# Kernel optimization log

Measured on AMD Instinct MI355X. Metric: run time of the kernel, lower is better.

## Reference

```python
import jax, jax.numpy as jnp
import numpy as np

E = 576        # embed_dims
HEADS = 18
NPTS = 12
NF = 3         # num_frames
DD = 2 * NF - 1  # depth of value volume (5)
HD = E // HEADS  # head dim (32)


def _grid_init_bias():
    # Faithful reproduction of init_weights() for sampling_offsets.bias
    theta = np.arange(8) * (2.0 * np.pi / 8)
    yaw = np.stack([np.cos(theta), np.sin(theta), np.zeros(8)], -1)
    roll = np.stack([np.zeros(8), np.cos(theta), np.sin(theta)], -1)
    pitch = np.stack([np.cos(theta), np.zeros(8), np.sin(theta)], -1)
    g = np.concatenate([yaw, pitch[[1, 2, 3, 5, 6, 7]], roll[[1, 3, 5, 7]]], 0)  # (18,3)
    g = g / np.abs(g).max(-1, keepdims=True)
    g = np.tile(g[:, None, None, :], (1, 1, NPTS, 1))              # (18,1,12,3)
    g = g * np.arange(1, NPTS + 1, dtype=np.float64)[None, None, :, None]
    return g.reshape(-1).astype(np.float32)                        # (18*12*3,)


def setup_inputs() -> dict:
    key = jax.random.key(0)
    ks = jax.random.split(key, 6)
    bs, h, w = 2, 64, 80
    nq = h * w
    lim = float(np.sqrt(6.0 / (E + E)))  # xavier uniform for square E x E
    return {
        "query": jax.random.normal(ks[0], (bs, nq, E), jnp.float32),
        "value": jax.random.normal(ks[1], (bs, nq * DD, E), jnp.float32),
        "query_pos": jax.random.normal(ks[2], (bs, nq, E), jnp.float32),
        "W_off": jnp.zeros((E, HEADS * NPTS * 3), jnp.float32),  # constant_init 0
        "b_off": jnp.asarray(_grid_init_bias()),
        "W_attn": jnp.zeros((E, HEADS * NPTS), jnp.float32),
        "b_attn": jnp.zeros((HEADS * NPTS,), jnp.float32),
        "W_v": jax.random.uniform(ks[3], (E, E), jnp.float32, -lim, lim),
        "b_v": jnp.zeros((E,), jnp.float32),
        "W_out": jax.random.uniform(ks[4], (E, E), jnp.float32, -lim, lim),
        "b_out": jnp.zeros((E,), jnp.float32),
        "h": 64,
        "w": 80,
    }


def _deform_attn_3d(value, loc, attn, D, H, W):
    # value: (bs, D*H*W, heads, hd)  token order: depth-major (D, H, W)
    # loc:   (bs, nq, heads, np, 3)  normalized (x, y, z) in [0,1]
    # attn:  (bs, nq, heads, np)
    bs, _, heads, hd = value.shape
    nq = loc.shape[1]
    # (bs, heads, D*H*W, hd) flat spatial for gathers
    v = value.reshape(bs, D, H, W, heads, hd).transpose(0, 4, 1, 2, 3, 5)
    v = v.reshape(bs, heads, D * H * W, hd)
    lt = jnp.moveaxis(loc, 2, 1)    # (bs, heads, nq, np, 3)
    at = jnp.moveaxis(attn, 2, 1)   # (bs, heads, nq, np)
    # grid_sample(align_corners=False) coordinate convention: pix = u*size - 0.5
    x = lt[..., 0] * W - 0.5
    y = lt[..., 1] * H - 0.5
    z = lt[..., 2] * D - 0.5
    x0 = jnp.floor(x); y0 = jnp.floor(y); z0 = jnp.floor(z)
    fx = x - x0; fy = y - y0; fz = z - z0
    acc = jnp.zeros((bs, heads, nq, NPTS, hd), v.dtype)
    for dz in (0, 1):
        for dy in (0, 1):
            for dx in (0, 1):
                xi = x0 + dx; yi = y0 + dy; zi = z0 + dz
                wgt = ((fx if dx else 1.0 - fx)
                       * (fy if dy else 1.0 - fy)
                       * (fz if dz else 1.0 - fz))
                valid = ((xi >= 0) & (xi < W) & (yi >= 0) & (yi < H)
                         & (zi >= 0) & (zi < D))
                xc = jnp.clip(xi, 0, W - 1).astype(jnp.int32)
                yc = jnp.clip(yi, 0, H - 1).astype(jnp.int32)
                zc = jnp.clip(zi, 0, D - 1).astype(jnp.int32)
                idx = ((zc * H + yc) * W + xc).reshape(bs, heads, nq * NPTS)
                g = jnp.take_along_axis(v, idx[..., None], axis=2)
                g = g.reshape(bs, heads, nq, NPTS, hd)
                acc = acc + g * (wgt * valid.astype(v.dtype))[..., None]
    out = jnp.einsum("bhqp,bhqpd->bhqd", at, acc)  # softmax-weighted sum over points
    return out.transpose(0, 2, 1, 3).reshape(bs, nq, heads * hd)


def _forward(query, value, query_pos, W_off, b_off, W_attn, b_attn,
             W_v, b_v, W_out, b_out, h, w):
    bs, nq, _ = query.shape
    q = query + query_pos
    v = (value @ W_v + b_v).reshape(bs, nq * DD, HEADS, HD)
    offs = (q @ W_off + b_off).reshape(bs, nq, HEADS, NPTS, 3)
    attn = jax.nn.softmax((q @ W_attn + b_attn).reshape(bs, nq, HEADS, NPTS), axis=-1)
    # reference points: pixel centers normalized, z = 0
    ry, rx = jnp.meshgrid((jnp.arange(h, dtype=jnp.float32) + 0.5) / h,
                          (jnp.arange(w, dtype=jnp.float32) + 0.5) / w,
                          indexing="ij")
    ref = jnp.stack([rx.reshape(-1), ry.reshape(-1),
                     jnp.zeros(h * w, jnp.float32)], -1)  # (nq, 3)
    norm = jnp.array([w, h, NF], jnp.float32)  # NOTE: z normalized by num_frames (as in source)
    loc = ref[None, :, None, None, :] + offs / norm
    out = _deform_attn_3d(v, loc, attn, DD, h, w)
    return out @ W_out + b_out  # dropout is identity at eval


def reference(query, value, query_pos, W_off, b_off, W_attn, b_attn,
              W_v, b_v, W_out, b_out, h, w):
    return _forward(query, value, query_pos, W_off, b_off, W_attn, b_attn,
                    W_v, b_v, W_out, b_out, h, w)
```

## Files before the change

### kernel.cpp

```cpp
#include <hip/hip_runtime.h>
#include <cstdint>

#define E_DIM   576
#define HEADS   18
#define NPTS    12
#define DDEPTH  5
#define HDIM    32
#define BSZ     2
#define GH      64
#define GW      80
#define NQ      (GH*GW)
#define NTOK    (NQ*DDEPTH)
#define MIXW    864
#define BQ_TOT  (BSZ*NQ)

typedef __attribute__((ext_vector_type(8))) short short8;
typedef __attribute__((ext_vector_type(4))) float f32x4;

__device__ __forceinline__ float b2f_lo(uint32_t u) {
    union { uint32_t u; float f; } v; v.u = u << 16; return v.f;
}
__device__ __forceinline__ float b2f_hi(uint32_t u) {
    union { uint32_t u; float f; } v; v.u = u & 0xffff0000u; return v.f;
}
__device__ __forceinline__ ushort f2b(float f) {
    union { float f; uint32_t u; } v; v.f = f;
    return (ushort)((v.u + 0x7fffu + ((v.u >> 16) & 1u)) >> 16);
}

__global__ void prep_all(const float* __restrict__ value,
                         const float* __restrict__ query, const float* __restrict__ query_pos,
                         const float* __restrict__ W_v, const float* __restrict__ W_out,
                         const float* __restrict__ W_off, const float* __restrict__ W_attn,
                         const float* __restrict__ b_off, const float* __restrict__ b_attn,
                         ushort* __restrict__ val_bf16, ushort* __restrict__ q_bf16,
                         ushort* __restrict__ wt_v, ushort* __restrict__ wt_out,
                         ushort* __restrict__ wt_mix, float* __restrict__ bias_mix) {
    const int i = blockIdx.x * blockDim.x + threadIdx.x;
    if (i < 51200 * 576 / 4) {
        const float4 v = reinterpret_cast<const float4*>(value)[i];
        ushort4 o; o.x = f2b(v.x); o.y = f2b(v.y); o.z = f2b(v.z); o.w = f2b(v.w);
        reinterpret_cast<ushort4*>(val_bf16)[i] = o;
    }
    if (i < 10240 * 576 / 4) {
        const float4 va = reinterpret_cast<const float4*>(query)[i];
        const float4 vb = reinterpret_cast<const float4*>(query_pos)[i];
        ushort4 o;
        o.x = f2b(va.x + vb.x); o.y = f2b(va.y + vb.y);
        o.z = f2b(va.z + vb.z); o.w = f2b(va.w + vb.w);
        reinterpret_cast<ushort4*>(q_bf16)[i] = o;
    }
    if (i < 864) bias_mix[i] = (i < 648) ? b_off[i] : b_attn[i - 648];
    if (i < 331776) {
        int n = i / E_DIM, k = i - n * E_DIM;
        wt_v[i] = f2b(W_v[(size_t)k * E_DIM + n]);
    } else if (i < 663552) {
        int j = i - 331776;
        int n = j / E_DIM, k = j - n * E_DIM;
        wt_out[j] = f2b(W_out[(size_t)k * E_DIM + n]);
    } else if (i < 1161216) {
        int j = i - 663552;
        int n = j / E_DIM, k = j - n * E_DIM;
        float v = (n < 648) ? W_off[(size_t)k * 648 + n] : W_attn[(size_t)k * 216 + (n - 648)];
        wt_mix[j] = f2b(v);
    }
}

#define TM 128
#define TN 96
#define BK 32

__device__ __forceinline__ void async_cp16(const ushort* gsrc, ushort* ldst) {
    __builtin_amdgcn_global_load_lds(
        (const __attribute__((address_space(1))) void*)gsrc,
        (__attribute__((address_space(3))) void*)ldst, 16, 0, 0);
}

template <typename OutT>
__device__ __forceinline__ void gemm_body(ushort* __restrict__ smem, int bx, int by,
                                          const ushort* __restrict__ A,
                                          const ushort* __restrict__ Bt,
                                          const float* __restrict__ bias,
                                          OutT* __restrict__ C, int K, int ldc) {
    ushort* Asb = smem;
    ushort* Bsb = smem + TM * BK;
    const int tid  = threadIdx.x;
    const int wave = tid >> 6;
    const int lane = tid & 63;
    const int m16  = lane & 15;
    const int quad = lane >> 4;
    const int wr   = wave >> 1;
    const int wc   = wave & 1;
    const int row0 = bx * TM;
    const int n0   = by * TN;

    const f32x4 zero = {0.f, 0.f, 0.f, 0.f};
    f32x4 acc[4][3];
    #pragma unroll
    for (int rt = 0; rt < 4; ++rt)
        #pragma unroll
        for (int ct = 0; ct < 3; ++ct) acc[rt][ct] = zero;

    const int srow = lane >> 2;
    const int scol = (((lane & 3) ^ ((lane >> 3) & 3))) * 8;
    const int ksw  = (quad ^ ((m16 >> 1) & 3)) * 8;

    for (int k0 = 0; k0 < K; k0 += BK) {
        #pragma unroll
        for (int c = 0; c < 2; ++c) {
            const int ch = wave + c * 4;
            async_cp16(A + (size_t)(row0 + ch * 16 + srow) * K + k0 + scol,
                       Asb + ch * 512 + lane * 8);
        }
        async_cp16(Bt + (size_t)(n0 + wave * 16 + srow) * K + k0 + scol,
                   Bsb + wave * 512 + lane * 8);
        if (wave < 2)
            async_cp16(Bt + (size_t)(n0 + (wave + 4) * 16 + srow) * K + k0 + scol,
                       Bsb + (wave + 4) * 512 + lane * 8);
        __syncthreads();

        short8 afrag[4], bfrag[3];
        #pragma unroll
        for (int rt = 0; rt < 4; ++rt)
            afrag[rt] = *reinterpret_cast<const short8*>(
                Asb + (wr * 4 + rt) * 512 + m16 * 32 + ksw);
        #pragma unroll
        for (int ct = 0; ct < 3; ++ct)
            bfrag[ct] = *reinterpret_cast<const short8*>(
                Bsb + (wc * 3 + ct) * 512 + m16 * 32 + ksw);

        #pragma unroll
        for (int rt = 0; rt < 4; ++rt)
            #pragma unroll
            for (int ct = 0; ct < 3; ++ct)
                acc[rt][ct] = __builtin_amdgcn_mfma_f32_16x16x32_bf16(
                    afrag[rt], bfrag[ct], acc[rt][ct], 0, 0, 0);

        __syncthreads();
    }

    #pragma unroll
    for (int ct = 0; ct < 3; ++ct) {
        const int col = n0 + wc * 48 + ct * 16 + m16;
        const float bcol = bias[col];
        #pragma unroll
        for (int rt = 0; rt < 4; ++rt) {
            #pragma unroll
            for (int r = 0; r < 4; ++r) {
                const int row = row0 + wr * 64 + rt * 16 + quad * 4 + r;
                const float val = acc[rt][ct][r] + bcol;
                if constexpr (__is_same(OutT, float)) {
                    C[(size_t)row * ldc + col] = val;
                } else {
                    C[(size_t)row * ldc + col] = f2b(val);
                }
            }
        }
    }
}

template <typename OutT>
__global__ void gemm_mfma(const ushort* __restrict__ A, const ushort* __restrict__ Bt,
                          const float* __restrict__ bias, OutT* __restrict__ C,
                          int K, int ldc) {
    __shared__ __align__(16) ushort smem[(TM + TN) * BK];
    gemm_body<OutT>(smem, blockIdx.x, blockIdx.y, A, Bt, bias, C, K, ldc);
}

__global__ void gemm_dual(const ushort* __restrict__ A1, const ushort* __restrict__ B1,
                          const float* __restrict__ bias1, float* __restrict__ C1,
                          int K1, int ldc1, int nbx1, int split,
                          const ushort* __restrict__ A2, const ushort* __restrict__ B2,
                          const float* __restrict__ bias2, ushort* __restrict__ C2,
                          int K2, int ldc2, int nbx2) {
    __shared__ __align__(16) ushort smem[(TM + TN) * BK];
    const int id = blockIdx.x;
    if (id < split) {
        gemm_body<float>(smem, id % nbx1, id / nbx1, A1, B1, bias1, C1, K1, ldc1);
    } else {
        const int j = id - split;
        gemm_body<ushort>(smem, j % nbx2, j / nbx2, A2, B2, bias2, C2, K2, ldc2);
    }
}

__global__ void __launch_bounds__(256, 8)
deform_kernel(const ushort* __restrict__ vbuf,
              const float* __restrict__ mix,
              ushort* __restrict__ aout) {
    __shared__ uint2 corn[16 * NPTS * 8];
    __shared__ uint32_t cmask[16 * NPTS];
    const int gl   = threadIdx.x >> 4;
    const int l    = threadIdx.x & 15;
    const int head = blockIdx.x / 640;
    const int bq   = (blockIdx.x % 640) * 16 + gl;
    const int q    = bq % NQ;
    const int b    = bq / NQ;
    const int qx   = q % GW;
    const int qy   = q / GW;

    const float* mrow = mix + (size_t)bq * MIXW;

    float lg = (l < NPTS) ? mrow[648 + head * NPTS + l] : -1e30f;
    float mx = lg;
    #pragma unroll
    for (int mk = 1; mk < 16; mk <<= 1) mx = fmaxf(mx, __shfl_xor(mx, mk, 16));
    float e = (l < NPTS) ? __expf(lg - mx) : 0.f;
    float s = e;
    #pragma unroll
    for (int mk = 1; mk < 16; mk <<= 1) s += __shfl_xor(s, mk, 16);

    float    cw[8];
    uint32_t coff[8];
    uint32_t mask = 0;
    {
        const float ap = e / s;
        const int pl = (l < NPTS) ? l : 0;
        const int ob = (head * NPTS + pl) * 3;
        const float ox = mrow[ob + 0];
        const float oy = mrow[ob + 1];
        const float oz = mrow[ob + 2];
        const float x = (float)qx + ox;
        const float y = (float)qy + oy;
        const float z = oz * (5.0f / 3.0f) - 0.5f;
        const float x0f = floorf(x), y0f = floorf(y), z0f = floorf(z);
        const int x0 = (int)x0f, y0 = (int)y0f, z0 = (int)z0f;
        const float fx = x - x0f, fy = y - y0f, fz = z - z0f;

        #pragma unroll
        for (int dz = 0; dz < 2; ++dz) {
            const int zi = z0 + dz;
            const bool zv = (zi >= 0) & (zi < DDEPTH);
            const int zc = min(max(zi, 0), DDEPTH - 1);
            const float wz = dz ? fz : 1.f - fz;
            #pragma unroll
            for (int dy = 0; dy < 2; ++dy) {
                const int yi = y0 + dy;
                const bool yv = (yi >= 0) & (yi < GH);
                const int yc = min(max(yi, 0), GH - 1);
                const float wy = dy ? fy : 1.f - fy;
                #pragma unroll
                for (int dx = 0; dx < 2; ++dx) {
                    const int xi = x0 + dx;
                    const bool xv = (xi >= 0) & (xi < GW);
                    const int xc = min(max(xi, 0), GW - 1);
                    const float wx = dx ? fx : 1.f - fx;
                    const int i = dz * 4 + dy * 2 + dx;
                    const bool valid = zv & yv & xv & (l < NPTS);
                    cw[i]   = ap * wz * wy * wx;
                    coff[i] = (uint32_t)((zc * GH + yc) * GW + xc) * (E_DIM / 2);
                    mask |= (valid ? (1u << i) : 0u);
                }
            }
        }
    }

    if (l < NPTS) {
        cmask[gl * NPTS + l] = mask;
        uint4* dst = reinterpret_cast<uint4*>(&corn[(gl * NPTS + l) * 8]);
        #pragma unroll
        for (int i2 = 0; i2 < 4; ++i2) {
            uint4 w;
            w.x = __float_as_uint(cw[2 * i2]);     w.y = coff[2 * i2];
            w.z = __float_as_uint(cw[2 * i2 + 1]); w.w = coff[2 * i2 + 1];
            dst[i2] = w;
        }
    }
    __syncthreads();

    const uint32_t* vb = reinterpret_cast<const uint32_t*>(vbuf)
                         + (size_t)b * NTOK * (E_DIM / 2) + head * (HDIM / 2) + l;
    const uint2* cg = &corn[gl * NPTS * 8];
    float o0 = 0.f, o1 = 0.f;
    for (int p = 0; p < NPTS; ++p) {
        const uint32_t msk = cmask[gl * NPTS + p];
        if (msk == 0) continue;
        #pragma unroll
        for (int i = 0; i < 8; ++i) {
            if (msk & (1u << i)) {
                const uint2 wo = cg[p * 8 + i];
                const float w = __uint_as_float(wo.x);
                const uint32_t pair = vb[wo.y];
                o0 += w * b2f_lo(pair);
                o1 += w * b2f_hi(pair);
            }
        }
    }
    const uint32_t packed = (uint32_t)f2b(o0) | ((uint32_t)f2b(o1) << 16);
    reinterpret_cast<uint32_t*>(aout)[(size_t)bq * (E_DIM / 2) + head * (HDIM / 2) + l] = packed;
}

extern "C" void kernel_launch(void* const* d_in, const int* in_sizes, int n_in,
                              void* d_out, int out_size, void* d_ws, size_t ws_size,
                              hipStream_t stream) {
    const float* query     = (const float*)d_in[0];
    const float* value     = (const float*)d_in[1];
    const float* query_pos = (const float*)d_in[2];
    const float* W_off     = (const float*)d_in[3];
    const float* b_off     = (const float*)d_in[4];
    const float* W_attn    = (const float*)d_in[5];
    const float* b_attn    = (const float*)d_in[6];
    const float* W_v       = (const float*)d_in[7];
    const float* b_v       = (const float*)d_in[8];
    const float* W_out     = (const float*)d_in[9];
    const float* b_out     = (const float*)d_in[10];
    float* out = (float*)d_out;

    char* ws = (char*)d_ws;
    ushort* vbuf     = (ushort*)(ws);
    ushort* val_bf16 = (ushort*)(ws + 58982400);
    ushort* aout     = val_bf16;
    ushort* q_bf16   = (ushort*)(ws + 117964800);
    float*  mixb     = (float*) (ws + 129761280);
    ushort* wt_v     = (ushort*)(ws + 165150720);
    ushort* wt_out   = (ushort*)(ws + 165814272);
    ushort* wt_mix   = (ushort*)(ws + 166477824);
    float*  bias_mix = (float*) (ws + 167473152);

    prep_all<<<(51200 * 576 / 4) / 256, 256, 0, stream>>>(
        value, query, query_pos, W_v, W_out, W_off, W_attn, b_off, b_attn,
        val_bf16, q_bf16, wt_v, wt_out, wt_mix, bias_mix);

    gemm_dual<<<720 + 2400, 256, 0, stream>>>(
        q_bf16, wt_mix, bias_mix, mixb, E_DIM, MIXW, BQ_TOT / TM, 720,
        val_bf16, wt_v, b_v, vbuf, E_DIM, E_DIM, (BSZ * NTOK) / TM);

    deform_kernel<<<HEADS * 640, 256, 0, stream>>>(vbuf, mixb, aout);

    gemm_mfma<float><<<dim3(BQ_TOT / TM, E_DIM / TN), 256, 0, stream>>>(
        aout, wt_out, b_out, out, E_DIM, E_DIM);
}
```

Measured before the change: 396.1 us.

## Remap GEMM blocks per XCD and compact valid deform corners into dense list

GEMM block indices are remapped so that consecutive logical tiles, which share the same A row panel across N tiles, land on the same XCD. The goal is better L2 reuse on the multi-die GPU. The deform kernel now prefix-sums the per-point valid-corner counts across the 16 lanes and writes only valid corners into a compacted shared-memory list, so the gather loop runs over a dense count with no per-bit mask checks. The mapping assumes the total block count is divisible by 8, and the compaction adds shuffle work before the barrier.

```diff
diff --git a/kernel.cpp b/kernel.cpp
--- a/kernel.cpp
+++ b/kernel.cpp
@@ -74,6 +74,14 @@
     __builtin_amdgcn_global_load_lds(
         (const __attribute__((address_space(1))) void*)gsrc,
         (__attribute__((address_space(3))) void*)ldst, 16, 0, 0);
+}
+
+__device__ __forceinline__ void xcd_map(int id, int total, int nbn, int& bx, int& by) {
+    const int xcd = id & 7;
+    const int pos = id >> 3;
+    const int logical = xcd * (total >> 3) + pos;
+    by = logical % nbn;
+    bx = logical / nbn;
 }
 
 template <typename OutT>
@@ -162,24 +170,28 @@
 template <typename OutT>
 __global__ void gemm_mfma(const ushort* __restrict__ A, const ushort* __restrict__ Bt,
                           const float* __restrict__ bias, OutT* __restrict__ C,
-                          int K, int ldc) {
+                          int K, int ldc, int total, int nbn) {
     __shared__ __align__(16) ushort smem[(TM + TN) * BK];
-    gemm_body<OutT>(smem, blockIdx.x, blockIdx.y, A, Bt, bias, C, K, ldc);
+    int bx, by;
+    xcd_map(blockIdx.x, total, nbn, bx, by);
+    gemm_body<OutT>(smem, bx, by, A, Bt, bias, C, K, ldc);
 }
 
 __global__ void gemm_dual(const ushort* __restrict__ A1, const ushort* __restrict__ B1,
                           const float* __restrict__ bias1, float* __restrict__ C1,
-                          int K1, int ldc1, int nbx1, int split,
+                          int K1, int ldc1, int nbn1, int split,
                           const ushort* __restrict__ A2, const ushort* __restrict__ B2,
                           const float* __restrict__ bias2, ushort* __restrict__ C2,
-                          int K2, int ldc2, int nbx2) {
+                          int K2, int ldc2, int nbn2, int total2) {
     __shared__ __align__(16) ushort smem[(TM + TN) * BK];
     const int id = blockIdx.x;
+    int bx, by;
     if (id < split) {
-        gemm_body<float>(smem, id % nbx1, id / nbx1, A1, B1, bias1, C1, K1, ldc1);
+        xcd_map(id, split, nbn1, bx, by);
+        gemm_body<float>(smem, bx, by, A1, B1, bias1, C1, K1, ldc1);
     } else {
-        const int j = id - split;
-        gemm_body<ushort>(smem, j % nbx2, j / nbx2, A2, B2, bias2, C2, K2, ldc2);
+        xcd_map(id - split, total2, nbn2, bx, by);
+        gemm_body<ushort>(smem, bx, by, A2, B2, bias2, C2, K2, ldc2);
     }
 }
 
@@ -187,8 +199,8 @@
 deform_kernel(const ushort* __restrict__ vbuf,
               const float* __restrict__ mix,
               ushort* __restrict__ aout) {
-    __shared__ uint2 corn[16 * NPTS * 8];
-    __shared__ uint32_t cmask[16 * NPTS];
+    __shared__ uint2 corn[16 * 97];
+    __shared__ int   ccnt[16];
     const int gl   = threadIdx.x >> 4;
     const int l    = threadIdx.x & 15;
     const int head = blockIdx.x / 640;
@@ -254,36 +266,38 @@
         }
     }
 
-    if (l < NPTS) {
-        cmask[gl * NPTS + l] = mask;
-        uint4* dst = reinterpret_cast<uint4*>(&corn[(gl * NPTS + l) * 8]);
-        #pragma unroll
-        for (int i2 = 0; i2 < 4; ++i2) {
-            uint4 w;
-            w.x = __float_as_uint(cw[2 * i2]);     w.y = coff[2 * i2];
-            w.z = __float_as_uint(cw[2 * i2 + 1]); w.w = coff[2 * i2 + 1];
-            dst[i2] = w;
+    const int cnt = __popc(mask);
+    int pre = cnt;
+    #pragma unroll
+    for (int mk = 1; mk < 16; mk <<= 1) {
+        const int t = __shfl_up(pre, mk, 16);
+        if (l >= mk) pre += t;
+    }
+    int o = gl * 97 + (pre - cnt);
+    #pragma unroll
+    for (int i = 0; i < 8; ++i) {
+        if (mask & (1u << i)) {
+            uint2 w; w.x = __float_as_uint(cw[i]); w.y = coff[i];
+            corn[o] = w;
+            ++o;
         }
     }
+    if (l == 15) ccnt[gl] = pre;
     __syncthreads();
 
-    const uint32_t* vb = reinterpret_cast<const uint32_t*>(vbuf)
-                         + (size_t)b * NTOK * (E_DIM / 2) + head * (HDIM / 2) + l;
-    const uint2* cg = &corn[gl * NPTS * 8];
+    const uint32_t lbase = (uint32_t)b * (uint32_t)(NTOK * (E_DIM / 2))
+                         + (uint32_t)(head * (HDIM / 2) + l);
+    const uint32_t* vb32 = reinterpret_cast<const uint32_t*>(vbuf);
+    const int n = ccnt[gl];
+    const uint2* cg = &corn[gl * 97];
     float o0 = 0.f, o1 = 0.f;
-    for (int p = 0; p < NPTS; ++p) {
-        const uint32_t msk = cmask[gl * NPTS + p];
-        if (msk == 0) continue;
-        #pragma unroll
-        for (int i = 0; i < 8; ++i) {
-            if (msk & (1u << i)) {
-                const uint2 wo = cg[p * 8 + i];
-                const float w = __uint_as_float(wo.x);
-                const uint32_t pair = vb[wo.y];
-                o0 += w * b2f_lo(pair);
-                o1 += w * b2f_hi(pair);
-            }
-        }
+    #pragma unroll 2
+    for (int j = 0; j < n; ++j) {
+        const uint2 wo = cg[j];
+        const uint32_t pair = vb32[lbase + wo.y];
+        const float w = __uint_as_float(wo.x);
+        o0 += w * b2f_lo(pair);
+        o1 += w * b2f_hi(pair);
     }
     const uint32_t packed = (uint32_t)f2b(o0) | ((uint32_t)f2b(o1) << 16);
     reinterpret_cast<uint32_t*>(aout)[(size_t)bq * (E_DIM / 2) + head * (HDIM / 2) + l] = packed;
@@ -321,11 +335,11 @@
         val_bf16, q_bf16, wt_v, wt_out, wt_mix, bias_mix);
 
     gemm_dual<<<720 + 2400, 256, 0, stream>>>(
-        q_bf16, wt_mix, bias_mix, mixb, E_DIM, MIXW, BQ_TOT / TM, 720,
-        val_bf16, wt_v, b_v, vbuf, E_DIM, E_DIM, (BSZ * NTOK) / TM);
+        q_bf16, wt_mix, bias_mix, mixb, E_DIM, MIXW, 9, 720,
+        val_bf16, wt_v, b_v, vbuf, E_DIM, E_DIM, 6, 2400);
 
     deform_kernel<<<HEADS * 640, 256, 0, stream>>>(vbuf, mixb, aout);
 
-    gemm_mfma<float><<<dim3(BQ_TOT / TM, E_DIM / TN), 256, 0, stream>>>(
-        aout, wt_out, b_out, out, E_DIM, E_DIM);
-}
+    gemm_mfma<float><<<480, 256, 0, stream>>>(
+        aout, wt_out, b_out, out, E_DIM, E_DIM, 480, 6);
+}
```

Result: faster. 357.5 us (-9.8%).
